# Optimization experiments

Hardware: AMD Instinct MI355X
Metric: run time of the kernel (lower is better)

The kernel has to match this reference:

```python
import jax, jax.numpy as jnp
import numpy as np

I2 = 256   # 2 * input_size
H2 = 256   # 2 * h_size
B, N, M = 64, 1024, 1024


def setup_inputs() -> dict:
    key = jax.random.key(0)
    ks = jax.random.split(key, 12)
    s_i2 = 1.0 / np.sqrt(I2)
    s_h2 = 1.0 / np.sqrt(H2)
    s_4i = 1.0 / np.sqrt(2 * I2)
    return {
        "up": jax.random.normal(ks[0], (B, N, I2), dtype=jnp.float32),
        "uq": jax.random.normal(ks[1], (B, M, I2), dtype=jnp.float32),
        # module-internal randn tensors, made explicit for determinism
        "v0": jax.random.normal(ks[2], (B, H2), dtype=jnp.float32),
        "V": jax.random.normal(ks[3], (B, H2, 1), dtype=jnp.float32),
        # linear weights, torch Linear convention y = x @ W.T, W: [out, in]
        "Wp": jax.random.normal(ks[4], (H2, I2), dtype=jnp.float32) * s_i2,
        "Wq": jax.random.normal(ks[5], (H2, I2), dtype=jnp.float32) * s_i2,
        "Wv": jax.random.normal(ks[6], (H2, H2), dtype=jnp.float32) * s_h2,
        "Wg": jax.random.normal(ks[7], (2 * I2, 2 * I2), dtype=jnp.float32) * s_4i,
        # GRUCell params: gates ordered (r, z, n)
        "w_ih": jax.random.normal(ks[8], (3 * H2, I2), dtype=jnp.float32) * s_h2,
        "w_hh": jax.random.normal(ks[9], (3 * H2, H2), dtype=jnp.float32) * s_h2,
        "b_ih": jax.random.normal(ks[10], (3 * H2,), dtype=jnp.float32) * s_h2,
        "b_hh": jax.random.normal(ks[11], (3 * H2,), dtype=jnp.float32) * s_h2,
    }


def _gru_cell(x, h, w_ih, w_hh, b_ih, b_hh):
    gi = x @ w_ih.T + b_ih          # [b, 3H]
    gh = h @ w_hh.T + b_hh          # [b, 3H]
    i_r, i_z, i_n = jnp.split(gi, 3, axis=1)
    h_r, h_z, h_n = jnp.split(gh, 3, axis=1)
    r = jax.nn.sigmoid(i_r + h_r)
    z = jax.nn.sigmoid(i_z + h_z)
    n = jnp.tanh(i_n + r * h_n)
    return (1.0 - z) * n + z * h


def reference(up, uq, v0, V, Wp, Wq, Wv, Wg, w_ih, w_hh, b_ih, b_hh):
    # up: [b, n, 2i], uq: [b, m, 2i]
    Up = jnp.transpose(up, (1, 0, 2))       # [n, b, 2i]
    Uq = jnp.transpose(uq, (1, 0, 2))       # [m, b, 2i]
    Uq_ = uq                                 # [b, m, 2i]
    Wuq = Uq @ Wq.T                          # [m, b, 2h] (loop-invariant)
    Vv = V[:, :, 0]                          # [b, 2h]

    def step(v, up_i):
        x = jnp.tanh(up_i @ Wp.T + Wuq + v @ Wv.T)       # [m, b, 2h]
        s = jnp.einsum('mbh,bh->bm', x, Vv)               # attention scores
        a = jax.nn.softmax(s, axis=1)                     # [b, m]
        c = jnp.einsum('bm,bmi->bi', a, Uq_)              # [b, 2i]
        r = jnp.concatenate([up_i, c], axis=1)            # [b, 4i]
        g = jax.nn.sigmoid(r @ Wg.T)
        c_ = (g * r)[:, I2:]                              # gated context [b, 2i]
        v_new = _gru_cell(c_, v, w_ih, w_hh, b_ih, b_hh)
        return v_new, v_new

    _, vs = jax.lax.scan(step, v0, Up)       # vs: [n, b, 2h]
    return vs  # dropout with p=0 is identity
```

## Files before the change

### kernel.cpp

```cpp
#include <hip/hip_runtime.h>

#define Bn 64
#define Nn 1024
#define Mn 1024
#define GSTR 16384
#define KSCALE 2.8853900817779268f

typedef unsigned short u16;
typedef _Float16 h2 __attribute__((ext_vector_type(2)));

__device__ __forceinline__ float us2f(u16 u) {
    _Float16 h = __builtin_bit_cast(_Float16, u);
    return (float)h;
}
__device__ __forceinline__ u16 f2h(float f) {
    _Float16 h = (_Float16)f;
    return __builtin_bit_cast(u16, h);
}
__device__ __forceinline__ float rcp_fast(float x) {
#if __has_builtin(__builtin_amdgcn_rcpf)
    return __builtin_amdgcn_rcpf(x);
#else
    return 1.0f / x;
#endif
}
__device__ __forceinline__ float exp2_fast(float x) {
#if __has_builtin(__builtin_amdgcn_exp2f)
    return __builtin_amdgcn_exp2f(x);
#else
    return exp2f(x);
#endif
}
__device__ __forceinline__ float wsum(float x) {
#pragma unroll
    for (int m = 32; m > 0; m >>= 1) x += __shfl_xor(x, m, 64);
    return x;
}
__device__ __forceinline__ float wmax(float x) {
#pragma unroll
    for (int m = 32; m > 0; m >>= 1) x = fmaxf(x, __shfl_xor(x, m, 64));
    return x;
}
__device__ __forceinline__ float dot2(unsigned a, unsigned b, float c) {
#if __has_builtin(__builtin_amdgcn_fdot2)
    return __builtin_amdgcn_fdot2(__builtin_bit_cast(h2, a), __builtin_bit_cast(h2, b), c, false);
#else
    h2 av = __builtin_bit_cast(h2, a), bv = __builtin_bit_cast(h2, b);
    return c + (float)av.x * (float)bv.x + (float)av.y * (float)bv.y;
#endif
}
__device__ __forceinline__ void agst(float* p, float v) {
    __hip_atomic_store(p, v, __ATOMIC_RELAXED, __HIP_MEMORY_SCOPE_AGENT);
}
__device__ __forceinline__ float agld(float* p) {
    return __hip_atomic_load(p, __ATOMIC_RELAXED, __HIP_MEMORY_SCOPE_AGENT);
}
__device__ __forceinline__ void agstu(unsigned* p, unsigned v) {
    __hip_atomic_store(p, v, __ATOMIC_RELAXED, __HIP_MEMORY_SCOPE_AGENT);
}
__device__ __forceinline__ unsigned agldu(unsigned* p) {
    return __hip_atomic_load(p, __ATOMIC_RELAXED, __HIP_MEMORY_SCOPE_AGENT);
}

__global__ __launch_bounds__(256)
void gemm_f16(const float* __restrict__ U, const float* __restrict__ W,
              u16* __restrict__ outN, u16* __restrict__ outT,
              int transposed, float scale) {
    __shared__ float WL[256 * 33];
    __shared__ float uL[32 * 33];
    const int tid = threadIdx.x;
    const size_t row0 = (size_t)blockIdx.x * 32;
    float acc[32];
#pragma unroll
    for (int m = 0; m < 32; ++m) acc[m] = 0.f;
    for (int ic = 0; ic < 8; ++ic) {
        __syncthreads();
        for (int e = tid; e < 8192; e += 256) {
            int h = e >> 5, ii = e & 31;
            WL[h * 33 + ii] = W[h * 256 + ic * 32 + ii];
        }
        for (int e = tid; e < 1024; e += 256) {
            int r = e >> 5, ii = e & 31;
            uL[r * 33 + ii] = U[(row0 + r) * 256 + ic * 32 + ii];
        }
        __syncthreads();
#pragma unroll 4
        for (int ii = 0; ii < 32; ++ii) {
            float w = WL[tid * 33 + ii];
#pragma unroll
            for (int m = 0; m < 32; ++m)
                acc[m] = fmaf(w, uL[m * 33 + ii], acc[m]);
        }
    }
    if (!transposed) {
#pragma unroll
        for (int m = 0; m < 32; ++m)
            outN[(row0 + m) * 256 + tid] = f2h(scale * acc[m]);
    } else {
        __syncthreads();
#pragma unroll
        for (int m = 0; m < 32; ++m) WL[tid * 33 + m] = acc[m];
        __syncthreads();
        const size_t batch = row0 >> 10;
        const int m0 = (int)(row0 & 1023);
        for (int e = tid; e < 8192; e += 256) {
            int h = e >> 5, mm = e & 31;
            outT[(batch * 256 + h) * 1024 + m0 + mm] = f2h(scale * WL[h * 33 + mm]);
        }
    }
}

__global__ void pack8(const float* __restrict__ src, u16* __restrict__ dst,
                      int R, int C, float scale) {
    int idx = blockIdx.x * blockDim.x + threadIdx.x;
    int total = R * (C >> 3);
    if (idx >= total) return;
    int c8 = idx / R, r = idx - c8 * R;
    u16 pk[8];
#pragma unroll
    for (int e = 0; e < 8; ++e) pk[e] = f2h(scale * src[(size_t)r * C + c8 * 8 + e]);
    *(uint4*)&dst[(size_t)idx * 8] = *(uint4*)pk;
}

__global__ __launch_bounds__(256)
void uq_pack(const float* __restrict__ uq, u16* __restrict__ out) {
    __shared__ float T[32][65];
    const int blk = blockIdx.x;
    const int ib = blk & 3, mt = (blk >> 2) & 31, b = blk >> 7;
    const int tid = threadIdx.x;
#pragma unroll
    for (int s = 0; s < 8; ++s) {
        int idx = tid + 256 * s, mm = idx >> 6, ii = idx & 63;
        T[mm][ii] = uq[((size_t)b * 1024 + mt * 32 + mm) * 256 + ib * 64 + ii];
    }
    __syncthreads();
    const int mo = tid >> 6, ii = tid & 63;
    u16 pk[8];
#pragma unroll
    for (int e = 0; e < 8; ++e) pk[e] = f2h(T[mo * 8 + e][ii]);
    *(uint4*)&out[(((size_t)b * 128 + mt * 4 + mo) * 256 + ib * 64 + ii) * 8] = *(uint4*)pk;
}

__global__ __launch_bounds__(1024, 4)
void scan_kernel(const float* __restrict__ up, const float* __restrict__ v0,
                 const float* __restrict__ V, const float* __restrict__ b_ih,
                 const float* __restrict__ b_hh,
                 const u16* __restrict__ WuqT, const u16* __restrict__ Pm,
                 const u16* __restrict__ uqP, const u16* __restrict__ WvP,
                 const u16* __restrict__ wihP, const u16* __restrict__ whhP,
                 const u16* __restrict__ Wg2P,
                 float* __restrict__ out, unsigned int* __restrict__ ctrs,
                 float* __restrict__ gdata) {
    const int tid = threadIdx.x;
    const int bid = blockIdx.x;
    const int x = bid & 7, q = (bid >> 3) & 3, bhi = bid >> 5;
    const int b = (bhi << 3) | x;

    unsigned int* ctr = ctrs + b * 16;
    float* gb = gdata + (size_t)b * GSTR;
    float* cpartF = gb;
    float* mlsB   = gb + 1024;
    unsigned* gpkB = (unsigned*)(gb + 1032);

    __shared__ __align__(16) u16 WuqL[256 * 256];
    __shared__ __align__(16) float scratch[2048];
    __shared__ __align__(16) float2 dvLds[256];
    __shared__ __align__(16) float vLds[256], pnLds[256];
    __shared__ __align__(16) u16 eH[256], rH[512], vHu[256], cH[64];
    __shared__ __align__(16) float bihs[768], bhhs[768];
    __shared__ float red[32];
    __shared__ float svv_sh;

    {
        const unsigned* src32 = (const unsigned*)(WuqT + (size_t)b * 256 * 1024);
        unsigned* dst32 = (unsigned*)WuqL;
        for (int d = tid; d < 32768; d += 1024) {
            int h = d >> 7, mp = d & 127;
            dst32[d] = src32[h * 512 + q * 128 + mp];
        }
    }
    if (tid < 768) { bihs[tid] = b_ih[tid]; bhhs[tid] = b_hh[tid]; }
    float vvreg = 0.f;
    if (tid < 256) {
        float v = v0[b * 256 + tid];
        vLds[tid] = v;
        vHu[tid] = f2h(v);
        vvreg = 2.0f * V[b * 256 + tid];
        pnLds[tid] = us2f(Pm[(size_t)b * Nn * 256 + tid]);
    }
    __syncthreads();
    {
        float s = wsum(vvreg);
        if ((tid & 63) == 0) red[tid >> 6] = s;
    }
    {
        const int h = tid & 255, jc = tid >> 8;
        const uint4* wv = (const uint4*)WvP;
        const unsigned* vH32 = (const unsigned*)vHu;
        float acc = 0.f;
#pragma unroll
        for (int l = 0; l < 8; ++l) {
            uint4 Wd = wv[(size_t)(jc * 8 + l) * 256 + h];
            int vb = jc * 32 + l * 4;
            acc = dot2(Wd.x, vH32[vb + 0], acc);
            acc = dot2(Wd.y, vH32[vb + 1], acc);
            acc = dot2(Wd.z, vH32[vb + 2], acc);
            acc = dot2(Wd.w, vH32[vb + 3], acc);
        }
        scratch[jc * 256 + h] = acc;
    }
    __syncthreads();
    if (tid == 0) svv_sh = 0.5f * (red[0] + red[1] + red[2] + red[3]);
    if (tid < 256)
        dvLds[tid] = make_float2(pnLds[tid] + scratch[tid] + scratch[256 + tid] +
                                 scratch[512 + tid] + scratch[768 + tid], vvreg);
    __syncthreads();
    const float SVv = svv_sh;

    const uint4* uqP_b = (const uint4*)(uqP + (size_t)b * 128 * 256 * 8);
    const float* up_b = up + (size_t)b * Nn * 256;

    long long budget = 1LL << 26;
    float mloc, sumloc;

    for (int t = 0; t < Nn; ++t) {
        const int iD = tid & 255, mcD = tid >> 8;
        const uint4* uqrow = uqP_b + (size_t)(q * 32 + mcD * 8) * 256 + iD;
        uint4 U0 = uqrow[0 * 256], U1 = uqrow[1 * 256];
        uint4 U2 = uqrow[2 * 256], U3 = uqrow[3 * 256];
        uint4 U4 = uqrow[4 * 256], U5 = uqrow[5 * 256];
        uint4 U6 = uqrow[6 * 256], U7 = uqrow[7 * 256];
        __builtin_amdgcn_sched_barrier(0);

        {
            const int m2 = (tid & 127) * 2;
            const int hc = tid >> 7;
            float a0 = 0.f, a1 = 0.f;
            const u16* wrow = &WuqL[(hc * 32) * 256 + m2];
#pragma unroll 8
            for (int hh = 0; hh < 32; ++hh) {
                float2 dv = dvLds[hc * 32 + hh];
                unsigned w2 = *(const unsigned*)wrow;
                wrow += 256;
                float w0 = us2f((u16)(w2 & 0xffffu));
                float w1 = us2f((u16)(w2 >> 16));
                a0 = fmaf(dv.y, rcp_fast(1.f + exp2_fast(w0 + dv.x)), a0);
                a1 = fmaf(dv.y, rcp_fast(1.f + exp2_fast(w1 + dv.x)), a1);
            }
            ((float2*)scratch)[hc * 128 + (tid & 127)] = make_float2(a0, a1);
        }
        __syncthreads();

        {
            const int m = tid & 255;
            float sv = SVv;
#pragma unroll
            for (int c2 = 0; c2 < 8; ++c2) sv -= scratch[c2 * 256 + m];
            if (tid >= 256) sv = -3.0e38f;
            float mx = wmax(sv);
            if ((tid & 63) == 0) red[tid >> 6] = mx;
            __syncthreads();
            mloc = red[0];
#pragma unroll
            for (int w2 = 1; w2 < 16; ++w2) mloc = fmaxf(mloc, red[w2]);
            float ev = __expf(sv - mloc);
            if (tid < 256) eH[m] = f2h(ev);
            float sm = wsum(ev);
            if ((tid & 63) == 0) red[16 + (tid >> 6)] = sm;
            __syncthreads();
            sumloc = red[16] + red[17] + red[18] + red[19];
        }

        {
            const unsigned* eH32 = (const unsigned*)eH;
            float acc = 0.f;
            int eb = mcD * 32;
            acc = dot2(U0.x, eH32[eb + 0], acc);  acc = dot2(U0.y, eH32[eb + 1], acc);
            acc = dot2(U0.z, eH32[eb + 2], acc);  acc = dot2(U0.w, eH32[eb + 3], acc);
            acc = dot2(U1.x, eH32[eb + 4], acc);  acc = dot2(U1.y, eH32[eb + 5], acc);
            acc = dot2(U1.z, eH32[eb + 6], acc);  acc = dot2(U1.w, eH32[eb + 7], acc);
            acc = dot2(U2.x, eH32[eb + 8], acc);  acc = dot2(U2.y, eH32[eb + 9], acc);
            acc = dot2(U2.z, eH32[eb + 10], acc); acc = dot2(U2.w, eH32[eb + 11], acc);
            acc = dot2(U3.x, eH32[eb + 12], acc); acc = dot2(U3.y, eH32[eb + 13], acc);
            acc = dot2(U3.z, eH32[eb + 14], acc); acc = dot2(U3.w, eH32[eb + 15], acc);
            acc = dot2(U4.x, eH32[eb + 16], acc); acc = dot2(U4.y, eH32[eb + 17], acc);
            acc = dot2(U4.z, eH32[eb + 18], acc); acc = dot2(U4.w, eH32[eb + 19], acc);
            acc = dot2(U5.x, eH32[eb + 20], acc); acc = dot2(U5.y, eH32[eb + 21], acc);
            acc = dot2(U5.z, eH32[eb + 22], acc); acc = dot2(U5.w, eH32[eb + 23], acc);
            acc = dot2(U6.x, eH32[eb + 24], acc); acc = dot2(U6.y, eH32[eb + 25], acc);
            acc = dot2(U6.z, eH32[eb + 26], acc); acc = dot2(U6.w, eH32[eb + 27], acc);
            acc = dot2(U7.x, eH32[eb + 28], acc); acc = dot2(U7.y, eH32[eb + 29], acc);
            acc = dot2(U7.z, eH32[eb + 30], acc); acc = dot2(U7.w, eH32[eb + 31], acc);
            scratch[mcD * 256 + iD] = acc;
        }
        __syncthreads();
        float upv = 0.f;
        if (tid < 256) {
            agst(&cpartF[q * 256 + tid], scratch[tid] + scratch[256 + tid] +
                                         scratch[512 + tid] + scratch[768 + tid]);
            upv = up_b[(size_t)t * 256 + tid];
        }
        if (tid == 0) { agst(&mlsB[2 * q], mloc); agst(&mlsB[2 * q + 1], sumloc); }
        __syncthreads();

        if (tid == 0) {
            asm volatile("s_waitcnt vmcnt(0)" ::: "memory");
            __hip_atomic_fetch_add(ctr + 0, 1u, __ATOMIC_RELAXED, __HIP_MEMORY_SCOPE_AGENT);
        }
        float ghv = 0.f;
        if (tid < 768) {
            const uint4* wh = (const uint4*)whhP;
            const unsigned* vH32 = (const unsigned*)vHu;
#pragma unroll
            for (int l = 0; l < 8; ++l) {
                uint4 Hd = wh[(size_t)(q * 8 + l) * 768 + tid];
                int vb = q * 32 + l * 4;
                ghv = dot2(Hd.x, vH32[vb + 0], ghv);
                ghv = dot2(Hd.y, vH32[vb + 1], ghv);
                ghv = dot2(Hd.z, vH32[vb + 2], ghv);
                ghv = dot2(Hd.w, vH32[vb + 3], ghv);
            }
        }
        if (tid == 0) {
            unsigned target = 4u * (unsigned)(t + 1);
            while (__hip_atomic_load(ctr + 0, __ATOMIC_RELAXED, __HIP_MEMORY_SCOPE_AGENT) < target) {
                __builtin_amdgcn_s_sleep(1);
                if (--budget < 0) break;
            }
        }
        __syncthreads();

        {
            if (tid < 8) red[tid] = agld(&mlsB[tid]);
            float cp0 = 0.f, cp1 = 0.f, cp2 = 0.f, cp3 = 0.f;
            if (tid < 256) {
                cp0 = agld(&cpartF[tid]);       cp1 = agld(&cpartF[256 + tid]);
                cp2 = agld(&cpartF[512 + tid]); cp3 = agld(&cpartF[768 + tid]);
            }
            __syncthreads();
            if (tid < 256) {
                float m0 = red[0], s0 = red[1], m1 = red[2], s1 = red[3];
                float m2 = red[4], s2 = red[5], m3 = red[6], s3 = red[7];
                float Mg = fmaxf(fmaxf(m0, m1), fmaxf(m2, m3));
                float w0 = __expf(m0 - Mg), w1 = __expf(m1 - Mg);
                float w2 = __expf(m2 - Mg), w3 = __expf(m3 - Mg);
                float denom = s0 * w0 + s1 * w1 + s2 * w2 + s3 * w3;
                float c = cp0 * w0 + cp1 * w1 + cp2 * w2 + cp3 * w3;
                c *= rcp_fast(denom);
                rH[tid] = f2h(upv);
                rH[256 + tid] = f2h(c);
            }
            __syncthreads();
        }

        {
            const int o = tid & 63, ks = tid >> 6;
            const uint4* wg = (const uint4*)Wg2P;
            const unsigned* rH32 = (const unsigned*)rH;
            float acc = 0.f;
#pragma unroll
            for (int l = 0; l < 4; ++l) {
                int k8 = ks * 4 + l;
                uint4 Wd = wg[(size_t)k8 * 256 + q * 64 + o];
                int kb = k8 * 4;
                acc = dot2(Wd.x, rH32[kb + 0], acc);
                acc = dot2(Wd.y, rH32[kb + 1], acc);
                acc = dot2(Wd.z, rH32[kb + 2], acc);
                acc = dot2(Wd.w, rH32[kb + 3], acc);
            }
            scratch[ks * 64 + o] = acc;
        }
        __syncthreads();
        if (tid < 64) {
            float acc = 0.f;
#pragma unroll
            for (int c2 = 0; c2 < 16; ++c2) acc += scratch[c2 * 64 + tid];
            float g = rcp_fast(1.f + __expf(-acc));
            cH[tid] = f2h(g * us2f(rH[256 + 64 * q + tid]));
        }
        __syncthreads();

        if (tid < 768) {
            const uint4* wi = (const uint4*)wihP;
            const unsigned* cH32 = (const unsigned*)cH;
            float gi = 0.f;
#pragma unroll
            for (int l = 0; l < 8; ++l) {
                uint4 Wd = wi[(size_t)(q * 8 + l) * 768 + tid];
                int kb = l * 4;
                gi = dot2(Wd.x, cH32[kb + 0], gi);
                gi = dot2(Wd.y, cH32[kb + 1], gi);
                gi = dot2(Wd.z, cH32[kb + 2], gi);
                gi = dot2(Wd.w, cH32[kb + 3], gi);
            }
            unsigned pk = (unsigned)f2h(gi) | ((unsigned)f2h(ghv) << 16);
            agstu(&gpkB[q * 768 + tid], pk);
        } else if (t + 1 < Nn) {
            const int h = tid - 768;
            pnLds[h] = us2f(Pm[((size_t)b * Nn + t + 1) * 256 + h]);
        }
        __syncthreads();

        if (tid == 0) {
            asm volatile("s_waitcnt vmcnt(0)" ::: "memory");
            __hip_atomic_fetch_add(ctr + 1, 1u, __ATOMIC_RELAXED, __HIP_MEMORY_SCOPE_AGENT);
            unsigned target = 4u * (unsigned)(t + 1);
            while (__hip_atomic_load(ctr + 1, __ATOMIC_RELAXED, __HIP_MEMORY_SCOPE_AGENT) < target) {
                __builtin_amdgcn_s_sleep(1);
                if (--budget < 0) break;
            }
        }
        __syncthreads();

        if (tid < 256) {
            const int h = tid;
            float gir = bihs[h], giz = bihs[256 + h], gin = bihs[512 + h];
            float ghr = bhhs[h], ghz = bhhs[256 + h], ghn = bhhs[512 + h];
#pragma unroll
            for (int s = 0; s < 4; ++s) {
                unsigned* gp = &gpkB[s * 768];
                unsigned p0 = agldu(&gp[h]);
                unsigned p1 = agldu(&gp[256 + h]);
                unsigned p2 = agldu(&gp[512 + h]);
                gir += us2f((u16)(p0 & 0xffffu)); ghr += us2f((u16)(p0 >> 16));
                giz += us2f((u16)(p1 & 0xffffu)); ghz += us2f((u16)(p1 >> 16));
                gin += us2f((u16)(p2 & 0xffffu)); ghn += us2f((u16)(p2 >> 16));
            }
            float rr = rcp_fast(1.f + __expf(-(gir + ghr)));
            float zz = rcp_fast(1.f + __expf(-(giz + ghz)));
            float narg = gin + rr * ghn;
            float nn = 1.f - 2.f * rcp_fast(1.f + __expf(2.f * narg));
            float vnew = (1.f - zz) * nn + zz * vLds[h];
            if ((h >> 6) == q) out[((size_t)t * Bn + b) * 256 + h] = vnew;
            vLds[h] = vnew;
            vHu[h] = f2h(vnew);
        }
        __syncthreads();

        if (t + 1 < Nn) {
            {
                const int h = tid & 255, jc = tid >> 8;
                const uint4* wv = (const uint4*)WvP;
                const unsigned* vH32 = (const unsigned*)vHu;
                float acc = 0.f;
#pragma unroll
                for (int l = 0; l < 8; ++l) {
                    uint4 Wd = wv[(size_t)(jc * 8 + l) * 256 + h];
                    int vb = jc * 32 + l * 4;
                    acc = dot2(Wd.x, vH32[vb + 0], acc);
                    acc = dot2(Wd.y, vH32[vb + 1], acc);
                    acc = dot2(Wd.z, vH32[vb + 2], acc);
                    acc = dot2(Wd.w, vH32[vb + 3], acc);
                }
                scratch[jc * 256 + h] = acc;
            }
            __syncthreads();
            if (tid < 256)
                dvLds[tid] = make_float2(pnLds[tid] + scratch[tid] + scratch[256 + tid] +
                                         scratch[512 + tid] + scratch[768 + tid], vvreg);
            __syncthreads();
        }
    }
}

extern "C" void kernel_launch(void* const* d_in, const int* in_sizes, int n_in,
                              void* d_out, int out_size, void* d_ws, size_t ws_size,
                              hipStream_t stream) {
    const float* up   = (const float*)d_in[0];
    const float* uq   = (const float*)d_in[1];
    const float* v0   = (const float*)d_in[2];
    const float* V    = (const float*)d_in[3];
    const float* Wp   = (const float*)d_in[4];
    const float* Wq   = (const float*)d_in[5];
    const float* Wv   = (const float*)d_in[6];
    const float* Wg   = (const float*)d_in[7];
    const float* w_ih = (const float*)d_in[8];
    const float* w_hh = (const float*)d_in[9];
    const float* b_ih = (const float*)d_in[10];
    const float* b_hh = (const float*)d_in[11];
    float* out = (float*)d_out;

    char* ws = (char*)d_ws;
    unsigned int* ctrs = (unsigned int*)ws;
    float* gdata = (float*)(ws + 8192);
    u16* WuqT = (u16*)(ws + (size_t)(8u << 20));
    u16* Pm   = WuqT + (size_t)Bn * 256 * 1024;
    u16* uqP  = Pm + (size_t)Bn * Nn * 256;
    u16* WvP  = uqP + (size_t)Bn * 128 * 256 * 8;
    u16* wihP = WvP + 65536;
    u16* whhP = wihP + 196608;
    u16* Wg2P = whhP + 196608;

    hipMemsetAsync(ctrs, 0, 4096, stream);

    hipLaunchKernelGGL(gemm_f16, dim3(2048), dim3(256), 0, stream,
                       uq, Wq, (u16*)nullptr, WuqT, 1, KSCALE);
    hipLaunchKernelGGL(gemm_f16, dim3(2048), dim3(256), 0, stream,
                       up, Wp, Pm, (u16*)nullptr, 0, KSCALE);
    hipLaunchKernelGGL(uq_pack, dim3(8192), dim3(256), 0, stream, uq, uqP);
    hipLaunchKernelGGL(pack8, dim3(32), dim3(256), 0, stream, Wv, WvP, 256, 256, KSCALE);
    hipLaunchKernelGGL(pack8, dim3(96), dim3(256), 0, stream, w_ih, wihP, 768, 256, 1.0f);
    hipLaunchKernelGGL(pack8, dim3(96), dim3(256), 0, stream, w_hh, whhP, 768, 256, 1.0f);
    hipLaunchKernelGGL(pack8, dim3(64), dim3(256), 0, stream, Wg + 512 * 256, Wg2P, 256, 512, 1.0f);

    hipLaunchKernelGGL(scan_kernel, dim3(256), dim3(1024), 0, stream,
                       up, v0, V, b_ih, b_hh,
                       WuqT, Pm, uqP, WvP, wihP, whhP, Wg2P,
                       out, ctrs, gdata);
}
```

Before: 25.11 ms.

## Compute full gated context per block and own GRU output slice, exchanging only new state

Each of the four blocks per batch now computes all 256 gated-context values, so it has the full input for its GRU gate rows. It then computes only its own 64 hidden units (192 gate rows split over 4 K-quarters) with row-major fp16 weights, instead of computing partial sums over a K-slice for all 768 rows. Those partial sums were previously packed and exchanged through global memory, and every block reduced all 256 units. Now only the 64 new state values per block are published, and each block reloads the full 256-element state before the Wv step. This cuts cross-block traffic and the redundant GRU math. In exchange each block does 4x the Wg matvec work and loads whole Wg/w_ih rows, and the synchronization ordering of the vnewF exchange must still be correct.

```diff
diff --git a/kernel.cpp b/kernel.cpp
--- a/kernel.cpp
+++ b/kernel.cpp
@@ -53,12 +53,6 @@
     __hip_atomic_store(p, v, __ATOMIC_RELAXED, __HIP_MEMORY_SCOPE_AGENT);
 }
 __device__ __forceinline__ float agld(float* p) {
-    return __hip_atomic_load(p, __ATOMIC_RELAXED, __HIP_MEMORY_SCOPE_AGENT);
-}
-__device__ __forceinline__ void agstu(unsigned* p, unsigned v) {
-    __hip_atomic_store(p, v, __ATOMIC_RELAXED, __HIP_MEMORY_SCOPE_AGENT);
-}
-__device__ __forceinline__ unsigned agldu(unsigned* p) {
     return __hip_atomic_load(p, __ATOMIC_RELAXED, __HIP_MEMORY_SCOPE_AGENT);
 }
 
@@ -122,6 +116,12 @@
     *(uint4*)&dst[(size_t)idx * 8] = *(uint4*)pk;
 }
 
+__global__ void cast_f16s(const float* __restrict__ src, u16* __restrict__ dst,
+                          int n, float scale) {
+    int i = blockIdx.x * blockDim.x + threadIdx.x;
+    if (i < n) dst[i] = f2h(scale * src[i]);
+}
+
 __global__ __launch_bounds__(256)
 void uq_pack(const float* __restrict__ uq, u16* __restrict__ out) {
     __shared__ float T[32][65];
@@ -147,8 +147,8 @@
                  const float* __restrict__ b_hh,
                  const u16* __restrict__ WuqT, const u16* __restrict__ Pm,
                  const u16* __restrict__ uqP, const u16* __restrict__ WvP,
-                 const u16* __restrict__ wihP, const u16* __restrict__ whhP,
-                 const u16* __restrict__ Wg2P,
+                 const u16* __restrict__ wih16, const u16* __restrict__ whh16,
+                 const u16* __restrict__ Wg216,
                  float* __restrict__ out, unsigned int* __restrict__ ctrs,
                  float* __restrict__ gdata) {
     const int tid = threadIdx.x;
@@ -160,14 +160,16 @@
     float* gb = gdata + (size_t)b * GSTR;
     float* cpartF = gb;
     float* mlsB   = gb + 1024;
-    unsigned* gpkB = (unsigned*)(gb + 1032);
+    float* vnewF  = gb + 1032;
 
     __shared__ __align__(16) u16 WuqL[256 * 256];
     __shared__ __align__(16) float scratch[2048];
+    __shared__ __align__(16) float giP[768], ghP[768];
     __shared__ __align__(16) float2 dvLds[256];
-    __shared__ __align__(16) float vLds[256], pnLds[256];
-    __shared__ __align__(16) u16 eH[256], rH[512], vHu[256], cH[64];
-    __shared__ __align__(16) float bihs[768], bhhs[768];
+    __shared__ __align__(16) float pnLds[256];
+    __shared__ __align__(16) u16 eH[256], rH[512], vHu[256], cH[256];
+    __shared__ __align__(16) float bihOwn[192], bhhOwn[192];
+    __shared__ float vOwn[64];
     __shared__ float red[32];
     __shared__ float svv_sh;
 
@@ -179,15 +181,19 @@
             dst32[d] = src32[h * 512 + q * 128 + mp];
         }
     }
-    if (tid < 768) { bihs[tid] = b_ih[tid]; bhhs[tid] = b_hh[tid]; }
+    if (tid < 192) {
+        int j = (tid >> 6) * 256 + q * 64 + (tid & 63);
+        bihOwn[tid] = b_ih[j];
+        bhhOwn[tid] = b_hh[j];
+    }
     float vvreg = 0.f;
     if (tid < 256) {
         float v = v0[b * 256 + tid];
-        vLds[tid] = v;
         vHu[tid] = f2h(v);
         vvreg = 2.0f * V[b * 256 + tid];
         pnLds[tid] = us2f(Pm[(size_t)b * Nn * 256 + tid]);
     }
+    if (tid < 64) vOwn[tid] = v0[b * 256 + q * 64 + tid];
     __syncthreads();
     {
         float s = wsum(vvreg);
@@ -230,6 +236,9 @@
         uint4 U2 = uqrow[2 * 256], U3 = uqrow[3 * 256];
         uint4 U4 = uqrow[4 * 256], U5 = uqrow[5 * 256];
         uint4 U6 = uqrow[6 * 256], U7 = uqrow[7 * 256];
+        float pnv = 0.f;
+        if (tid >= 768 && t + 1 < Nn)
+            pnv = us2f(Pm[((size_t)b * Nn + t + 1) * 256 + (tid - 768)]);
         __builtin_amdgcn_sched_barrier(0);
 
         {
@@ -307,19 +316,22 @@
             asm volatile("s_waitcnt vmcnt(0)" ::: "memory");
             __hip_atomic_fetch_add(ctr + 0, 1u, __ATOMIC_RELAXED, __HIP_MEMORY_SCOPE_AGENT);
         }
-        float ghv = 0.f;
         if (tid < 768) {
-            const uint4* wh = (const uint4*)whhP;
+            const int r = tid >> 2, kq = tid & 3;
+            const int j = (r >> 6) * 256 + q * 64 + (r & 63);
+            const uint4* wh = (const uint4*)(whh16 + (size_t)j * 256 + kq * 64);
             const unsigned* vH32 = (const unsigned*)vHu;
+            float gh = 0.f;
 #pragma unroll
             for (int l = 0; l < 8; ++l) {
-                uint4 Hd = wh[(size_t)(q * 8 + l) * 768 + tid];
-                int vb = q * 32 + l * 4;
-                ghv = dot2(Hd.x, vH32[vb + 0], ghv);
-                ghv = dot2(Hd.y, vH32[vb + 1], ghv);
-                ghv = dot2(Hd.z, vH32[vb + 2], ghv);
-                ghv = dot2(Hd.w, vH32[vb + 3], ghv);
-            }
+                uint4 Hd = wh[l];
+                int kb = kq * 32 + l * 4;
+                gh = dot2(Hd.x, vH32[kb + 0], gh);
+                gh = dot2(Hd.y, vH32[kb + 1], gh);
+                gh = dot2(Hd.z, vH32[kb + 2], gh);
+                gh = dot2(Hd.w, vH32[kb + 3], gh);
+            }
+            ghP[tid] = gh;
         }
         if (tid == 0) {
             unsigned target = 4u * (unsigned)(t + 1);
@@ -354,50 +366,71 @@
         }
 
         {
-            const int o = tid & 63, ks = tid >> 6;
-            const uint4* wg = (const uint4*)Wg2P;
+            const int o = tid >> 2, kq = tid & 3;
+            const uint4* wg = (const uint4*)(Wg216 + (size_t)o * 512 + kq * 128);
             const unsigned* rH32 = (const unsigned*)rH;
             float acc = 0.f;
 #pragma unroll
-            for (int l = 0; l < 4; ++l) {
-                int k8 = ks * 4 + l;
-                uint4 Wd = wg[(size_t)k8 * 256 + q * 64 + o];
-                int kb = k8 * 4;
+            for (int l = 0; l < 16; ++l) {
+                uint4 Wd = wg[l];
+                int kb = kq * 64 + l * 4;
                 acc = dot2(Wd.x, rH32[kb + 0], acc);
                 acc = dot2(Wd.y, rH32[kb + 1], acc);
                 acc = dot2(Wd.z, rH32[kb + 2], acc);
                 acc = dot2(Wd.w, rH32[kb + 3], acc);
             }
-            scratch[ks * 64 + o] = acc;
-        }
-        __syncthreads();
+            scratch[tid] = acc;
+        }
+        __syncthreads();
+        if (tid < 256) {
+            float acc = scratch[tid * 4] + scratch[tid * 4 + 1] +
+                        scratch[tid * 4 + 2] + scratch[tid * 4 + 3];
+            float g = rcp_fast(1.f + __expf(-acc));
+            cH[tid] = f2h(g * us2f(rH[256 + tid]));
+        }
+        __syncthreads();
+
+        if (tid < 768) {
+            const int r = tid >> 2, kq = tid & 3;
+            const int j = (r >> 6) * 256 + q * 64 + (r & 63);
+            const uint4* wi = (const uint4*)(wih16 + (size_t)j * 256 + kq * 64);
+            const unsigned* c32 = (const unsigned*)cH;
+            float gi = 0.f;
+#pragma unroll
+            for (int l = 0; l < 8; ++l) {
+                uint4 Wd = wi[l];
+                int kb = kq * 32 + l * 4;
+                gi = dot2(Wd.x, c32[kb + 0], gi);
+                gi = dot2(Wd.y, c32[kb + 1], gi);
+                gi = dot2(Wd.z, c32[kb + 2], gi);
+                gi = dot2(Wd.w, c32[kb + 3], gi);
+            }
+            giP[tid] = gi;
+        } else if (t + 1 < Nn) {
+            pnLds[tid - 768] = pnv;
+        }
+        __syncthreads();
+
         if (tid < 64) {
-            float acc = 0.f;
-#pragma unroll
-            for (int c2 = 0; c2 < 16; ++c2) acc += scratch[c2 * 64 + tid];
-            float g = rcp_fast(1.f + __expf(-acc));
-            cH[tid] = f2h(g * us2f(rH[256 + 64 * q + tid]));
-        }
-        __syncthreads();
-
-        if (tid < 768) {
-            const uint4* wi = (const uint4*)wihP;
-            const unsigned* cH32 = (const unsigned*)cH;
-            float gi = 0.f;
-#pragma unroll
-            for (int l = 0; l < 8; ++l) {
-                uint4 Wd = wi[(size_t)(q * 8 + l) * 768 + tid];
-                int kb = l * 4;
-                gi = dot2(Wd.x, cH32[kb + 0], gi);
-                gi = dot2(Wd.y, cH32[kb + 1], gi);
-                gi = dot2(Wd.z, cH32[kb + 2], gi);
-                gi = dot2(Wd.w, cH32[kb + 3], gi);
-            }
-            unsigned pk = (unsigned)f2h(gi) | ((unsigned)f2h(ghv) << 16);
-            agstu(&gpkB[q * 768 + tid], pk);
-        } else if (t + 1 < Nn) {
-            const int h = tid - 768;
-            pnLds[h] = us2f(Pm[((size_t)b * Nn + t + 1) * 256 + h]);
+            const int hl = tid;
+            float gir = giP[hl * 4] + giP[hl * 4 + 1] + giP[hl * 4 + 2] + giP[hl * 4 + 3] + bihOwn[hl];
+            float giz = giP[(64 + hl) * 4] + giP[(64 + hl) * 4 + 1] +
+                        giP[(64 + hl) * 4 + 2] + giP[(64 + hl) * 4 + 3] + bihOwn[64 + hl];
+            float gin = giP[(128 + hl) * 4] + giP[(128 + hl) * 4 + 1] +
+                        giP[(128 + hl) * 4 + 2] + giP[(128 + hl) * 4 + 3] + bihOwn[128 + hl];
+            float ghr = ghP[hl * 4] + ghP[hl * 4 + 1] + ghP[hl * 4 + 2] + ghP[hl * 4 + 3] + bhhOwn[hl];
+            float ghz = ghP[(64 + hl) * 4] + ghP[(64 + hl) * 4 + 1] +
+                        ghP[(64 + hl) * 4 + 2] + ghP[(64 + hl) * 4 + 3] + bhhOwn[64 + hl];
+            float ghn = ghP[(128 + hl) * 4] + ghP[(128 + hl) * 4 + 1] +
+                        ghP[(128 + hl) * 4 + 2] + ghP[(128 + hl) * 4 + 3] + bhhOwn[128 + hl];
+            float rr = rcp_fast(1.f + __expf(-(gir + ghr)));
+            float zz = rcp_fast(1.f + __expf(-(giz + ghz)));
+            float narg = gin + rr * ghn;
+            float nn = 1.f - 2.f * rcp_fast(1.f + __expf(2.f * narg));
+            float vnew = (1.f - zz) * nn + zz * vOwn[hl];
+            out[((size_t)t * Bn + b) * 256 + q * 64 + hl] = vnew;
+            vOwn[hl] = vnew;
+            agst(&vnewF[q * 64 + hl], vnew);
         }
         __syncthreads();
 
@@ -412,32 +445,9 @@
         }
         __syncthreads();
 
-        if (tid < 256) {
-            const int h = tid;
-            float gir = bihs[h], giz = bihs[256 + h], gin = bihs[512 + h];
-            float ghr = bhhs[h], ghz = bhhs[256 + h], ghn = bhhs[512 + h];
-#pragma unroll
-            for (int s = 0; s < 4; ++s) {
-                unsigned* gp = &gpkB[s * 768];
-                unsigned p0 = agldu(&gp[h]);
-                unsigned p1 = agldu(&gp[256 + h]);
-                unsigned p2 = agldu(&gp[512 + h]);
-                gir += us2f((u16)(p0 & 0xffffu)); ghr += us2f((u16)(p0 >> 16));
-                giz += us2f((u16)(p1 & 0xffffu)); ghz += us2f((u16)(p1 >> 16));
-                gin += us2f((u16)(p2 & 0xffffu)); ghn += us2f((u16)(p2 >> 16));
-            }
-            float rr = rcp_fast(1.f + __expf(-(gir + ghr)));
-            float zz = rcp_fast(1.f + __expf(-(giz + ghz)));
-            float narg = gin + rr * ghn;
-            float nn = 1.f - 2.f * rcp_fast(1.f + __expf(2.f * narg));
-            float vnew = (1.f - zz) * nn + zz * vLds[h];
-            if ((h >> 6) == q) out[((size_t)t * Bn + b) * 256 + h] = vnew;
-            vLds[h] = vnew;
-            vHu[h] = f2h(vnew);
-        }
-        __syncthreads();
-
         if (t + 1 < Nn) {
+            if (tid < 256) vHu[tid] = f2h(agld(&vnewF[tid]));
+            __syncthreads();
             {
                 const int h = tid & 255, jc = tid >> 8;
                 const uint4* wv = (const uint4*)WvP;
@@ -487,9 +497,9 @@
     u16* Pm   = WuqT + (size_t)Bn * 256 * 1024;
     u16* uqP  = Pm + (size_t)Bn * Nn * 256;
     u16* WvP  = uqP + (size_t)Bn * 128 * 256 * 8;
-    u16* wihP = WvP + 65536;
-    u16* whhP = wihP + 196608;
-    u16* Wg2P = whhP + 196608;
+    u16* wih16 = WvP + 65536;
+    u16* whh16 = wih16 + 196608;
+    u16* Wg216 = whh16 + 196608;
 
     hipMemsetAsync(ctrs, 0, 4096, stream);
 
@@ -499,12 +509,12 @@
                        up, Wp, Pm, (u16*)nullptr, 0, KSCALE);
     hipLaunchKernelGGL(uq_pack, dim3(8192), dim3(256), 0, stream, uq, uqP);
     hipLaunchKernelGGL(pack8, dim3(32), dim3(256), 0, stream, Wv, WvP, 256, 256, KSCALE);
-    hipLaunchKernelGGL(pack8, dim3(96), dim3(256), 0, stream, w_ih, wihP, 768, 256, 1.0f);
-    hipLaunchKernelGGL(pack8, dim3(96), dim3(256), 0, stream, w_hh, whhP, 768, 256, 1.0f);
-    hipLaunchKernelGGL(pack8, dim3(64), dim3(256), 0, stream, Wg + 512 * 256, Wg2P, 256, 512, 1.0f);
+    hipLaunchKernelGGL(cast_f16s, dim3(768), dim3(256), 0, stream, w_ih, wih16, 196608, 1.0f);
+    hipLaunchKernelGGL(cast_f16s, dim3(768), dim3(256), 0, stream, w_hh, whh16, 196608, 1.0f);
+    hipLaunchKernelGGL(cast_f16s, dim3(512), dim3(256), 0, stream, Wg + 512 * 256, Wg216, 131072, 1.0f);
 
     hipLaunchKernelGGL(scan_kernel, dim3(256), dim3(1024), 0, stream,
                        up, v0, V, b_ih, b_hh,
-                       WuqT, Pm, uqP, WvP, wihP, whhP, Wg2P,
+                       WuqT, Pm, uqP, WvP, wih16, whh16, Wg216,
                        out, ctrs, gdata);
 }
```

Measured after the change: 33.98 ms. +35.3%, slower.
